# Kernel optimization log

Measured on AMD Instinct MI355X. Metric: run time of the kernel, lower is better.

The kernel has to match this reference:

```python
import jax, jax.numpy as jnp
import numpy as np
import math

B, S, E, H = 2, 2048, 1024, 16
D = E // H  # d_attn = 64
SCALE = 1.0 / math.sqrt(D)


def setup_inputs() -> dict:
    key = jax.random.key(0)
    ks = jax.random.split(key, 5)
    std = 0.02
    return {
        "q": jax.random.normal(ks[0], (B, S, E), dtype=jnp.float32),
        "Wq": jax.random.normal(ks[1], (E, H * D), dtype=jnp.float32) * std,
        "Wk": jax.random.normal(ks[2], (E, H * D), dtype=jnp.float32) * std,
        "Wv": jax.random.normal(ks[3], (E, H * D), dtype=jnp.float32) * std,
        "Wo": jax.random.normal(ks[4], (H * D, E), dtype=jnp.float32) * std,
        "gamma": jnp.ones((H,), dtype=jnp.float32),
    }


def reference(q, Wq, Wk, Wv, Wo, gamma):
    Bq, Sq, _ = q.shape
    # projections -> [B, H, S, D]
    qh = (q @ Wq).reshape(Bq, Sq, H, D).transpose(0, 2, 1, 3)
    kh = (q @ Wk).reshape(Bq, Sq, H, D).transpose(0, 2, 1, 3)
    vh = (q @ Wv).reshape(Bq, Sq, H, D).transpose(0, 2, 1, 3)
    # RBF distance scores: ||q||^2 - 2 q.k + ||k||^2, clamped at 0
    q_norm = jnp.sum(qh * qh, axis=-1, keepdims=True)          # [B,H,S,1]
    k_norm = jnp.sum(kh * kh, axis=-1, keepdims=True)          # [B,H,S,1]
    qk = jnp.einsum("bhsd,bhtd->bhst", qh, kh)                # [B,H,S,S]
    dist = jnp.maximum(q_norm - 2.0 * qk + jnp.swapaxes(k_norm, -2, -1), 0.0)
    scores = jnp.exp(-gamma[None, :, None, None] * SCALE * dist)
    # source: masked_fill(causal_mask == 0, 0) with mask = triu(ones, 1)
    # -> scores kept only on the STRICT upper triangle (faithful to source)
    mask = jnp.triu(jnp.ones((Sq, Sq), dtype=bool), k=1)
    scores = jnp.where(mask, scores, 0.0)
    out = jnp.einsum("bhst,bhtd->bhsd", scores, vh)            # [B,H,S,D]
    out = out.transpose(0, 2, 1, 3).reshape(Bq, Sq, H * D)
    return out @ Wo
```

## Files before the change

### kernel.cpp

```cpp
#include <hip/hip_runtime.h>
#include <stdint.h>

#define SCALE 0.125f
#define GSL_C 0.180336880111f

typedef short s16x8 __attribute__((ext_vector_type(8)));
typedef float f32x4 __attribute__((ext_vector_type(4)));
typedef float f32x16 __attribute__((ext_vector_type(16)));

__device__ __forceinline__ unsigned short f2bf(float x){
  union { float f; unsigned int u; } v; v.f = x;
  unsigned int r = v.u + 0x7fffu + ((v.u >> 16) & 1u);
  return (unsigned short)(r >> 16);
}
__device__ __forceinline__ float bf2f(unsigned short u){
  union { unsigned int u; float f; } v; v.u = ((unsigned int)u) << 16;
  return v.f;
}
__device__ __forceinline__ f32x4 mfma16(s16x8 a, s16x8 b, f32x4 c){
  return __builtin_amdgcn_mfma_f32_16x16x32_bf16(a, b, c, 0, 0, 0);
}
__device__ __forceinline__ f32x16 mfma32(s16x8 a, s16x8 b, f32x16 c){
  return __builtin_amdgcn_mfma_f32_32x32x16_bf16(a, b, c, 0, 0, 0);
}
__device__ __forceinline__ void gld_lds16(const void* g, void* l){
  __builtin_amdgcn_global_load_lds(
      (const __attribute__((address_space(1))) unsigned int*)g,
      (__attribute__((address_space(3))) unsigned int*)l, 16, 0, 0);
}
__device__ __forceinline__ unsigned int cvtpk(float lo, float hi){
  unsigned int r;
  asm("v_cvt_pk_bf16_f32 %0, %1, %2" : "=v"(r) : "v"(lo), "v"(hi));
  return r;
}
__device__ __forceinline__ void plswap(unsigned int &a, unsigned int &b){
  asm("v_permlane32_swap_b32 %0, %1" : "+v"(a), "+v"(b));
}

__global__ __launch_bounds__(256) void prep_kernel(const float* __restrict__ in,
    unsigned short* __restrict__ out,
    const float* __restrict__ W0, const float* __restrict__ W1,
    const float* __restrict__ W2, const float* __restrict__ W3,
    unsigned short* __restrict__ Wt){
  int bid = blockIdx.x;
  int tid = threadIdx.x;
  if (bid < 2048){
    int i = bid*256 + tid;
    const float4* p = (const float4*)in + (size_t)i*2;
    float4 a = p[0], b = p[1];
    unsigned short t[8] = {f2bf(a.x),f2bf(a.y),f2bf(a.z),f2bf(a.w),
                           f2bf(b.x),f2bf(b.y),f2bf(b.z),f2bf(b.w)};
    *(s16x8*)(out + (size_t)i*8) = *(const s16x8*)t;
  } else {
    int idx = bid - 2048;
    int z = idx >> 8, rem = idx & 255;
    int k0 = (rem & 15)*64, n0 = (rem >> 4)*64;
    const float* src = (z==0)?W0:(z==1)?W1:(z==2)?W2:W3;
    unsigned short* dst = Wt + (size_t)z*1048576;
    __shared__ unsigned short tile[64*72];
    int r = tid>>2, c = (tid&3)*16;
    const float* p = src + (size_t)(k0+r)*1024 + n0 + c;
    #pragma unroll
    for (int j=0;j<16;j++) tile[r*72 + c + j] = f2bf(p[j]);
    __syncthreads();
    int n = tid>>2, kc = (tid&3)*16;
    unsigned short o[16];
    #pragma unroll
    for (int j=0;j<16;j++) o[j] = tile[(kc+j)*72 + n];
    *(s16x8*)&dst[(size_t)(n0+n)*1024 + k0 + kc]     = *(const s16x8*)o;
    *(s16x8*)&dst[(size_t)(n0+n)*1024 + k0 + kc + 8] = *(const s16x8*)(o+8);
  }
}

__global__ __launch_bounds__(256) void vtrans_kernel(const unsigned short* __restrict__ Vh,
    unsigned short* __restrict__ VtG){
  int bh = blockIdx.y, t0 = blockIdx.x*64;
  __shared__ unsigned short tile[64*72];
  int tid = threadIdx.x;
  #pragma unroll
  for (int p=0;p<2;p++){
    int idx = p*2048 + tid*8;
    int r = idx>>6, c = idx&63;
    *(s16x8*)&tile[r*72 + c] = *(const s16x8*)&Vh[((size_t)bh*2048 + t0 + r)*64 + c];
  }
  __syncthreads();
  #pragma unroll
  for (int p=0;p<2;p++){
    int idx = p*2048 + tid*8;
    int d = idx>>6, c = idx&63;
    unsigned short o[8];
    #pragma unroll
    for (int j=0;j<8;j++) o[j] = tile[(c+j)*72 + d];
    *(s16x8*)&VtG[((size_t)bh*64 + d)*2048 + t0 + c] = *(const s16x8*)o;
  }
}

template<int MODE>
__global__ __launch_bounds__(512) void gemm_db(const unsigned short* __restrict__ A,
    const unsigned short* __restrict__ Bt, unsigned short* __restrict__ outH,
    float* __restrict__ outF, float* __restrict__ qn, float* __restrict__ kn,
    const float* __restrict__ gamma){
  __shared__ short As[16384];
  __shared__ short Bs[16384];
  int tid = threadIdx.x;
  int w = tid>>6, l = tid&63;
  int lm = l & 15, hi = l >> 4;
  int wr = w>>1, wc = w&1;
  int m0 = blockIdx.x*128, n0 = blockIdx.y*128;

  const unsigned short* Bz;
  int bn0;
  if constexpr (MODE==1){ Bz = Bt + (size_t)(n0>>10)*1048576; bn0 = n0 & 1023; }
  else                  { Bz = Bt; bn0 = n0; }

  f32x4 acc[2][4];
  #pragma unroll
  for (int r=0;r<2;r++)
    #pragma unroll
    for (int c=0;c<4;c++){ f32x4 z = {0.f,0.f,0.f,0.f}; acc[r][c] = z; }

  int rsub = l>>3, csw = ((l&7) ^ (l>>3))*8;
  const unsigned short* gA = A  + (size_t)(m0  + w*16 + rsub)*1024 + csw;
  const unsigned short* gB = Bz + (size_t)(bn0 + w*16 + rsub)*1024 + csw;
  short* lA = As + w*1024;
  short* lB = Bs + w*1024;

  int ch0 = ((hi)     ^ (lm&7))*8;
  int ch1 = ((4 + hi) ^ (lm&7))*8;

  gld_lds16(gA,        lA);
  gld_lds16(gA + 8192, lA + 512);
  gld_lds16(gB,        lB);
  gld_lds16(gB + 8192, lB + 512);
  __syncthreads();

  const int NKT = 16;
  int buf = 0;
  for (int kt=0; kt<NKT; ++kt){
    if (kt+1 < NKT){
      const unsigned short* a = gA + (size_t)(kt+1)*64;
      const unsigned short* b = gB + (size_t)(kt+1)*64;
      short* dA = As + (buf^1)*8192 + w*1024;
      short* dB = Bs + (buf^1)*8192 + w*1024;
      gld_lds16(a,        dA);
      gld_lds16(a + 8192, dA + 512);
      gld_lds16(b,        dB);
      gld_lds16(b + 8192, dB + 512);
    }
    const short* curA = As + buf*8192;
    const short* curB = Bs + buf*8192;
    s16x8 af[2][2], bfv[4][2];
    #pragma unroll
    for (int r=0;r<2;r++){
      int ro = (wr*32 + r*16 + lm)*64;
      af[r][0] = *(const s16x8*)(curA + ro + ch0);
      af[r][1] = *(const s16x8*)(curA + ro + ch1);
    }
    #pragma unroll
    for (int c=0;c<4;c++){
      int ro = (wc*64 + c*16 + lm)*64;
      bfv[c][0] = *(const s16x8*)(curB + ro + ch0);
      bfv[c][1] = *(const s16x8*)(curB + ro + ch1);
    }
    __builtin_amdgcn_s_setprio(1);
    #pragma unroll
    for (int s=0;s<2;s++)
      #pragma unroll
      for (int r=0;r<2;r++)
        #pragma unroll
        for (int c=0;c<4;c++)
          acc[r][c] = mfma16(af[r][s], bfv[c][s], acc[r][c]);
    __builtin_amdgcn_s_setprio(0);
    __syncthreads();
    buf ^= 1;
  }

  if constexpr (MODE==0){
    #pragma unroll
    for (int r=0;r<2;r++)
      #pragma unroll
      for (int c=0;c<4;c++)
        #pragma unroll
        for (int i=0;i<4;i++){
          int m = m0 + wr*32 + r*16 + hi*4 + i;
          int n = n0 + wc*64 + c*16 + lm;
          outF[(size_t)m*1024 + n] = acc[r][c][i];
        }
  } else {
    int z = n0 >> 10;
    unsigned short* oz = outH + (size_t)z*4194304;
    #pragma unroll
    for (int r=0;r<2;r++){
      #pragma unroll
      for (int i=0;i<4;i++){
        int m = m0 + wr*32 + r*16 + hi*4 + i;
        int bq = m >> 11, sq = m & 2047;
        float nrm = 0.f;
        #pragma unroll
        for (int c=0;c<4;c++){
          int nn = (n0 & 1023) + wc*64 + c*16 + lm;
          int hq = nn >> 6, dq = nn & 63;
          int bh = bq*16 + hq;
          unsigned short bv = f2bf(acc[r][c][i]);
          oz[((size_t)bh*2048 + sq)*64 + dq] = bv;
          float vf = bf2f(bv);
          nrm = fmaf(vf, vf, nrm);
        }
        if (z < 2){
          nrm += __shfl_xor(nrm, 1);
          nrm += __shfl_xor(nrm, 2);
          nrm += __shfl_xor(nrm, 4);
          nrm += __shfl_xor(nrm, 8);
          if (lm == 0){
            int hq = ((n0 & 1023) + wc*64) >> 6;
            float gsl_h = gamma[hq] * GSL_C;
            float* dst = z ? kn : qn;
            dst[(size_t)(bq*16 + hq)*2048 + sq] = nrm * gsl_h;
          }
        }
      }
    }
  }
}

#define JOB(si,ts,te,buf,zm) ((unsigned int)((si)|((ts)<<4)|((te)<<10)|((buf)<<16)|((zm)<<18)))
__device__ const unsigned int JOBS[35] = {
  JOB(0,0,11,0,0),  JOB(0,11,22,1,0), JOB(0,22,32,2,0), JOB(1,2,12,0,0),
  JOB(1,12,22,1,0), JOB(1,22,32,2,0), JOB(2,4,14,0,0),  JOB(2,14,24,1,0),
  JOB(11,22,32,0,3),JOB(3,6,15,0,0),  JOB(3,15,24,1,0), JOB(2,24,32,2,0),
  JOB(3,24,32,2,0), JOB(4,8,16,0,0),  JOB(4,16,24,1,0), JOB(4,24,32,2,0),
  JOB(5,10,18,0,0), JOB(5,18,26,1,0), JOB(8,16,24,0,2), JOB(8,24,32,1,0),
  JOB(12,24,32,0,3),JOB(6,12,19,0,0), JOB(6,19,26,1,0), JOB(9,18,25,0,2),
  JOB(9,25,32,1,0), JOB(5,26,32,2,0), JOB(6,26,32,2,0), JOB(7,14,20,0,0),
  JOB(7,20,26,1,0), JOB(7,26,32,2,0), JOB(10,20,26,0,2),JOB(10,26,32,1,0),
  JOB(13,26,32,0,3),JOB(14,28,32,0,3),JOB(15,30,32,0,3)
};

__global__ __launch_bounds__(256, 4) void attn_kernel(const unsigned short* __restrict__ Qh,
    const unsigned short* __restrict__ Kh, const unsigned short* __restrict__ VtG,
    const float* __restrict__ qn, const float* __restrict__ kn,
    const float* __restrict__ gamma, unsigned short* __restrict__ aO0,
    unsigned short* __restrict__ aO1, unsigned short* __restrict__ aO2){
  __shared__ short Ks[2][4096];
  __shared__ short Vs[2][4096];

  int bid = blockIdx.x;
  int bh = bid & 31; int b = bh>>4, h = bh&15;
  unsigned int e = JOBS[bid >> 5];
  int si2 = e & 15, ts = (e>>4)&63, te = (e>>10)&63, bsel = (e>>16)&3, zm = (e>>18)&3;
  int s0 = si2*128;

  int tid = threadIdx.x, w = tid>>6, l = tid&63;
  int l31 = l & 31, hi5 = l >> 5, l7 = l & 7;
  float gs2l = 2.f * gamma[h] * GSL_C;

  int q0 = s0 + w*32;
  int qrow = q0 + l31;
  const unsigned short* qb = Qh + ((size_t)bh*2048 + qrow)*64;
  s16x8 qf[4];
  #pragma unroll
  for (int c=0;c<4;c++) qf[c] = *(const s16x8*)(qb + c*16 + hi5*8);
  float gq = -qn[(size_t)bh*2048 + qrow];
  const float* knp = kn + (size_t)bh*2048;

  int chs = (l7 ^ (l>>3))*8;
  const unsigned short* kp0 = Kh  + ((size_t)bh*2048 + w*8 + (l>>3))*64 + chs;
  const unsigned short* vp0 = VtG + ((size_t)bh*64 + w*8 + (l>>3))*2048 + chs;

  f32x16 accO0, accO1;
  #pragma unroll
  for (int r=0;r<16;r++){ accO0[r] = 0.f; accO1[r] = 0.f; }

#define STAGE(bufi, tabs) { \
    const unsigned short* kp = kp0 + (size_t)(tabs)*64; \
    const unsigned short* vp = vp0 + (tabs); \
    short* dK = &Ks[bufi][w*512]; \
    short* dV = &Vs[bufi][w*512]; \
    gld_lds16(kp,           dK); \
    gld_lds16(kp + 32*64,   dK + 2048); \
    gld_lds16(vp,           dV); \
    gld_lds16(vp + 32*2048, dV + 2048); \
  }

  STAGE(0, ts*64);
  __syncthreads();

  int cur = 0;
  for (int tt = ts; tt < te; ++tt, cur ^= 1){
    int t0 = tt*64;
    float4 kv[8];
    #pragma unroll
    for (int j=0;j<8;j++) kv[j] = *(const float4*)(knp + t0 + j*8 + hi5*4);
    if (tt + 1 < te) STAGE(cur^1, (tt+1)*64);
    const short* kb = &Ks[cur][0];
    const short* vb = &Vs[cur][0];

    #pragma unroll
    for (int tb=0; tb<2; tb++){
      int tbase = t0 + tb*32 - s0;
      if (tbase + 31 <= w*32) continue;
      f32x16 sc;
      #pragma unroll
      for (int r=0;r<16;r++) sc[r] = 0.f;
      __builtin_amdgcn_s_setprio(1);
      #pragma unroll
      for (int c=0;c<4;c++){
        s16x8 kf = *(const s16x8*)(kb + (tb*32 + l31)*64 + (((2*c + hi5) ^ l7)*8));
        sc = mfma32(kf, qf[c], sc);
      }
      __builtin_amdgcn_s_setprio(0);
      float ev[16];
      #pragma unroll
      for (int gg=0; gg<4; gg++){
        float4 knv = kv[tb*4 + gg];
        float ks4[4] = {knv.x, knv.y, knv.z, knv.w};
        #pragma unroll
        for (int i=0;i<4;i++){
          int r = gg*4 + i;
          ev[r] = __builtin_amdgcn_exp2f(fminf(fmaf(gs2l, sc[r], gq - ks4[i]), 0.f));
        }
      }
      if (tbase < w*32 + 32){
        #pragma unroll
        for (int r=0;r<16;r++){
          int t = t0 + tb*32 + (r&3) + 8*(r>>2) + 4*hi5;
          ev[r] = (t > qrow) ? ev[r] : 0.f;
        }
      }
      unsigned int u0 = cvtpk(ev[0],  ev[1]),  u1 = cvtpk(ev[2],  ev[3]);
      unsigned int u2 = cvtpk(ev[4],  ev[5]),  u3 = cvtpk(ev[6],  ev[7]);
      unsigned int u4 = cvtpk(ev[8],  ev[9]),  u5 = cvtpk(ev[10], ev[11]);
      unsigned int u6 = cvtpk(ev[12], ev[13]), u7 = cvtpk(ev[14], ev[15]);
      plswap(u0, u2);
      plswap(u1, u3);
      plswap(u4, u6);
      plswap(u5, u7);
      unsigned int f0[4] = {u0, u1, u2, u3};
      unsigned int f1[4] = {u4, u5, u6, u7};
      s16x8 pa0 = *(const s16x8*)f0;
      s16x8 pa1 = *(const s16x8*)f1;
      __builtin_amdgcn_s_setprio(1);
      {
        int cg0 = 2*tb, cg1 = 2*tb + 1;
        s16x8 v00 = *(const s16x8*)(vb + (l31)*64      + (((2*cg0 + hi5) ^ l7)*8));
        s16x8 v01 = *(const s16x8*)(vb + (l31)*64      + (((2*cg1 + hi5) ^ l7)*8));
        s16x8 v10 = *(const s16x8*)(vb + (32 + l31)*64 + (((2*cg0 + hi5) ^ l7)*8));
        s16x8 v11 = *(const s16x8*)(vb + (32 + l31)*64 + (((2*cg1 + hi5) ^ l7)*8));
        accO0 = mfma32(pa0, v00, accO0);
        accO0 = mfma32(pa1, v01, accO0);
        accO1 = mfma32(pa0, v10, accO1);
        accO1 = mfma32(pa1, v11, accO1);
      }
      __builtin_amdgcn_s_setprio(0);
    }
    __syncthreads();
  }
#undef STAGE

  unsigned short* aoP = (bsel==0) ? aO0 : (bsel==1) ? aO1 : aO2;
  #pragma unroll
  for (int r=0;r<16;r++){
    int s = q0 + (r&3) + 8*(r>>2) + 4*hi5;
    size_t base = ((size_t)b*2048 + s)*1024 + h*64;
    aoP[base + l31]      = f2bf(accO0[r]);
    aoP[base + 32 + l31] = f2bf(accO1[r]);
  }
  if (zm){
    s16x8 zz8 = {0,0,0,0,0,0,0,0};
    int zr = tid >> 1, zc = (tid & 1)*32;
    size_t zbase = ((size_t)b*2048 + s0 + zr)*1024 + h*64 + zc;
    if (zm & 1){
      #pragma unroll
      for (int j=0;j<4;j++) *(s16x8*)&aO1[zbase + j*8] = zz8;
    }
    if (zm & 2){
      #pragma unroll
      for (int j=0;j<4;j++) *(s16x8*)&aO2[zbase + j*8] = zz8;
    }
  }
}

__global__ __launch_bounds__(256) void sum3_kernel(unsigned short* __restrict__ a,
    const unsigned short* __restrict__ bsrc, const unsigned short* __restrict__ csrc){
  size_t i = ((size_t)blockIdx.x*256 + threadIdx.x)*8;
  s16x8 va = *(const s16x8*)(a + i);
  s16x8 vb = *(const s16x8*)(bsrc + i);
  s16x8 vc = *(const s16x8*)(csrc + i);
  unsigned short o[8];
  #pragma unroll
  for (int j=0;j<8;j++)
    o[j] = f2bf(bf2f((unsigned short)va[j]) + bf2f((unsigned short)vb[j])
                + bf2f((unsigned short)vc[j]));
  *(s16x8*)(a + i) = *(const s16x8*)o;
}

extern "C" void kernel_launch(void* const* d_in, const int* in_sizes, int n_in,
                              void* d_out, int out_size, void* d_ws, size_t ws_size,
                              hipStream_t stream){
  const float* q  = (const float*)d_in[0];
  const float* Wq = (const float*)d_in[1];
  const float* Wk = (const float*)d_in[2];
  const float* Wv = (const float*)d_in[3];
  const float* Wo = (const float*)d_in[4];
  const float* gm = (const float*)d_in[5];
  float* out = (float*)d_out;

  unsigned short* qbf = (unsigned short*)d_ws;
  unsigned short* Wt  = qbf + 4194304;
  unsigned short* Qh  = Wt  + 4194304;
  unsigned short* Kh  = Qh  + 4194304;
  unsigned short* Vh  = Kh  + 4194304;
  unsigned short* Vt  = Vh  + 4194304;
  unsigned short* aO  = Vt  + 4194304;
  float* qn = (float*)(aO + 4194304);
  float* kn = qn + 65536;

  unsigned short* aO1 = qbf;
  unsigned short* aO2 = Vh;

  prep_kernel  <<<dim3(3072), 256, 0, stream>>>(q, qbf, Wq, Wk, Wv, Wo, Wt);
  gemm_db<1>   <<<dim3(32,24), 512, 0, stream>>>(qbf, Wt, Qh, nullptr, qn, kn, gm);
  vtrans_kernel<<<dim3(32,32), 256, 0, stream>>>(Vh, Vt);
  attn_kernel  <<<dim3(1120), 256, 0, stream>>>(Qh, Kh, Vt, qn, kn, gm, aO, aO1, aO2);
  sum3_kernel  <<<dim3(2048), 256, 0, stream>>>(aO, aO1, aO2);
  gemm_db<0>   <<<dim3(32,8), 512, 0, stream>>>(aO, Wt + 3*1048576, nullptr, out, nullptr, nullptr, nullptr);
}
```

Baseline: 113.1 us.

## Rebalance attention job schedule and add smaller-tile output projection GEMM

Replaces the 35-entry attention work table with a 32-entry one, reducing the attention grid from 1120 to 1024 blocks and regrouping the causal tile ranges so the work splits more evenly. It also adds a dedicated output-projection GEMM with 128x64 tiles and a double-buffered LDS pipeline, launched as 512 blocks instead of the previous 256. The aim is better CU fill and less tail imbalance on the largest stages. The risk is that the new job table, with its changed accumulation modes, may cover or sum the output tiles differently, and that smaller GEMM tiles give less data reuse per block.

```diff
diff --git a/kernel.cpp b/kernel.cpp
--- a/kernel.cpp
+++ b/kernel.cpp
@@ -223,17 +223,94 @@
   }
 }
 
+__global__ __launch_bounds__(512) void gemm_out(const unsigned short* __restrict__ A,
+    const unsigned short* __restrict__ Bt, float* __restrict__ outF){
+  __shared__ short As[16384];
+  __shared__ short Bs[8192];
+  int tid = threadIdx.x;
+  int w = tid>>6, l = tid&63;
+  int lm = l & 15, hi = l >> 4;
+  int wr = w>>1, wc = w&1;
+  int m0 = blockIdx.x*128, n0 = blockIdx.y*64;
+
+  f32x4 acc[2][2];
+  #pragma unroll
+  for (int r=0;r<2;r++)
+    #pragma unroll
+    for (int c=0;c<2;c++){ f32x4 z = {0.f,0.f,0.f,0.f}; acc[r][c] = z; }
+
+  int rsub = l>>3, csw = ((l&7) ^ (l>>3))*8;
+  const unsigned short* gA = A  + (size_t)(m0 + w*16 + rsub)*1024 + csw;
+  const unsigned short* gB = Bt + (size_t)(n0 + w*8  + rsub)*1024 + csw;
+
+  int ch0 = ((hi)     ^ (lm&7))*8;
+  int ch1 = ((4 + hi) ^ (lm&7))*8;
+
+  gld_lds16(gA,        As + w*1024);
+  gld_lds16(gA + 8192, As + w*1024 + 512);
+  gld_lds16(gB,        Bs + w*512);
+  __syncthreads();
+
+  const int NKT = 16;
+  int buf = 0;
+  for (int kt=0; kt<NKT; ++kt){
+    if (kt+1 < NKT){
+      const unsigned short* a = gA + (size_t)(kt+1)*64;
+      const unsigned short* b = gB + (size_t)(kt+1)*64;
+      gld_lds16(a,        As + (buf^1)*8192 + w*1024);
+      gld_lds16(a + 8192, As + (buf^1)*8192 + w*1024 + 512);
+      gld_lds16(b,        Bs + (buf^1)*4096 + w*512);
+    }
+    const short* curA = As + buf*8192;
+    const short* curB = Bs + buf*4096;
+    s16x8 af[2][2], bfv[2][2];
+    #pragma unroll
+    for (int r=0;r<2;r++){
+      int ro = (wr*32 + r*16 + lm)*64;
+      af[r][0] = *(const s16x8*)(curA + ro + ch0);
+      af[r][1] = *(const s16x8*)(curA + ro + ch1);
+    }
+    #pragma unroll
+    for (int c=0;c<2;c++){
+      int ro = (wc*32 + c*16 + lm)*64;
+      bfv[c][0] = *(const s16x8*)(curB + ro + ch0);
+      bfv[c][1] = *(const s16x8*)(curB + ro + ch1);
+    }
+    __builtin_amdgcn_s_setprio(1);
+    #pragma unroll
+    for (int s=0;s<2;s++)
+      #pragma unroll
+      for (int r=0;r<2;r++)
+        #pragma unroll
+        for (int c=0;c<2;c++)
+          acc[r][c] = mfma16(af[r][s], bfv[c][s], acc[r][c]);
+    __builtin_amdgcn_s_setprio(0);
+    __syncthreads();
+    buf ^= 1;
+  }
+
+  #pragma unroll
+  for (int r=0;r<2;r++)
+    #pragma unroll
+    for (int c=0;c<2;c++)
+      #pragma unroll
+      for (int i=0;i<4;i++){
+        int m = m0 + wr*32 + r*16 + hi*4 + i;
+        int n = n0 + wc*32 + c*16 + lm;
+        outF[(size_t)m*1024 + n] = acc[r][c][i];
+      }
+}
+
 #define JOB(si,ts,te,buf,zm) ((unsigned int)((si)|((ts)<<4)|((te)<<10)|((buf)<<16)|((zm)<<18)))
-__device__ const unsigned int JOBS[35] = {
-  JOB(0,0,11,0,0),  JOB(0,11,22,1,0), JOB(0,22,32,2,0), JOB(1,2,12,0,0),
-  JOB(1,12,22,1,0), JOB(1,22,32,2,0), JOB(2,4,14,0,0),  JOB(2,14,24,1,0),
-  JOB(11,22,32,0,3),JOB(3,6,15,0,0),  JOB(3,15,24,1,0), JOB(2,24,32,2,0),
-  JOB(3,24,32,2,0), JOB(4,8,16,0,0),  JOB(4,16,24,1,0), JOB(4,24,32,2,0),
-  JOB(5,10,18,0,0), JOB(5,18,26,1,0), JOB(8,16,24,0,2), JOB(8,24,32,1,0),
-  JOB(12,24,32,0,3),JOB(6,12,19,0,0), JOB(6,19,26,1,0), JOB(9,18,25,0,2),
-  JOB(9,25,32,1,0), JOB(5,26,32,2,0), JOB(6,26,32,2,0), JOB(7,14,20,0,0),
-  JOB(7,20,26,1,0), JOB(7,26,32,2,0), JOB(10,20,26,0,2),JOB(10,26,32,1,0),
-  JOB(13,26,32,0,3),JOB(14,28,32,0,3),JOB(15,30,32,0,3)
+__device__ const unsigned int JOBS[32] = {
+  JOB(0,0,11,0,0),   JOB(5,10,21,0,0),  JOB(0,22,32,2,0),  JOB(1,12,22,1,0),
+  JOB(2,4,14,0,0),   JOB(6,22,32,1,2),  JOB(2,23,32,2,0),  JOB(7,14,23,0,0),
+  JOB(0,11,22,1,0),  JOB(5,21,32,1,2),  JOB(1,2,12,0,0),   JOB(1,22,32,2,0),
+  JOB(6,12,22,0,0),  JOB(2,14,23,1,0),  JOB(3,6,15,0,0),   JOB(7,23,32,1,2),
+  JOB(11,22,32,0,3), JOB(3,24,32,2,0),  JOB(4,8,16,0,0),   JOB(4,16,24,1,0),
+  JOB(4,24,32,2,0),  JOB(8,16,24,0,0),  JOB(3,15,24,1,0),  JOB(8,24,32,1,2),
+  JOB(15,30,32,0,3), JOB(14,28,32,0,3), JOB(10,20,26,0,0), JOB(10,26,32,1,2),
+  JOB(13,26,32,0,3), JOB(9,18,25,0,0),  JOB(9,25,32,1,2),  JOB(12,24,32,0,3)
 };
 
 __global__ __launch_bounds__(256, 4) void attn_kernel(const unsigned short* __restrict__ Qh,
@@ -421,7 +498,7 @@
   prep_kernel  <<<dim3(3072), 256, 0, stream>>>(q, qbf, Wq, Wk, Wv, Wo, Wt);
   gemm_db<1>   <<<dim3(32,24), 512, 0, stream>>>(qbf, Wt, Qh, nullptr, qn, kn, gm);
   vtrans_kernel<<<dim3(32,32), 256, 0, stream>>>(Vh, Vt);
-  attn_kernel  <<<dim3(1120), 256, 0, stream>>>(Qh, Kh, Vt, qn, kn, gm, aO, aO1, aO2);
+  attn_kernel  <<<dim3(1024), 256, 0, stream>>>(Qh, Kh, Vt, qn, kn, gm, aO, aO1, aO2);
   sum3_kernel  <<<dim3(2048), 256, 0, stream>>>(aO, aO1, aO2);
-  gemm_db<0>   <<<dim3(32,8), 512, 0, stream>>>(aO, Wt + 3*1048576, nullptr, out, nullptr, nullptr, nullptr);
-}
+  gemm_out     <<<dim3(32,16), 512, 0, stream>>>(aO, Wt + 3*1048576, out);
+}
```

Measured after the change: 106.1 us. -6.1%, faster.
